# Kernel tuning notes

Measured on AMD Instinct MI355X. Metric: run time of the kernel, lower is better.

Reference implementation:

```python
import jax, jax.numpy as jnp
import numpy as np

H = 16  # num heads
D = 64  # head dim


def rotate_half(x):
    h = x.shape[-1] // 2
    return jnp.concatenate([-x[..., h:], x[..., :h]], axis=-1)


def setup_inputs() -> dict:
    key = jax.random.key(0)
    ks = jax.random.split(key, 8)
    B, S, E = 2, 4096, 1024
    scale = 1.0 / np.sqrt(E)
    x = jax.random.normal(ks[0], (B, S, E), dtype=jnp.float32)
    Wq = jax.random.normal(ks[1], (E, E), dtype=jnp.float32) * scale
    Wk = jax.random.normal(ks[2], (E, E), dtype=jnp.float32) * scale
    Wv = jax.random.normal(ks[3], (E, E), dtype=jnp.float32) * scale
    Wg = jax.random.normal(ks[4], (E, E), dtype=jnp.float32) * scale
    Wo = jax.random.normal(ks[5], (E, E), dtype=jnp.float32) * scale
    cos = jax.random.normal(ks[6], (S, D), dtype=jnp.float32)
    sin = jax.random.normal(ks[7], (S, D), dtype=jnp.float32)
    return {"x": x, "Wq": Wq, "Wk": Wk, "Wv": Wv, "Wg": Wg, "Wo": Wo,
            "cos": cos, "sin": sin, "block_size": 256}


def reference(x, Wq, Wk, Wv, Wg, Wo, cos, sin, block_size):
    B, S, E = x.shape
    nb = S // block_size  # seq divisible by block_size (remainder==0 path)

    gate = (x @ Wg).reshape(B, S, H, D)
    q = (x @ Wq).reshape(B, S, H, D)
    k = (x @ Wk).reshape(B, S, H, D)
    v = (x @ Wv).reshape(B, S, H, D)

    # RoPE: cos/sin [S, D] -> broadcast over batch and heads (unsqueeze_dim=1 in torch
    # with [S, 1, D] after slicing gives the same broadcast over the head axis here).
    c = cos[:S][None, :, None, :]  # [1, S, 1, D]
    s = sin[:S][None, :, None, :]
    q = q * c + rotate_half(q) * s
    k = k * c + rotate_half(k) * s

    # Block-diagonal attention: reshape seq into blocks and attend within blocks only.
    def to_blocks(t):  # [B,S,H,D] -> [B,nb,H,block,D]
        return t.reshape(B, nb, block_size, H, D).transpose(0, 1, 3, 2, 4)

    qb, kb, vb = to_blocks(q), to_blocks(k), to_blocks(v)
    scores = jnp.einsum('bnhqd,bnhkd->bnhqk', qb, kb) / np.sqrt(D)
    attn = jax.nn.softmax(scores, axis=-1)
    ob = jnp.einsum('bnhqk,bnhkd->bnhqd', attn, vb)

    out = ob.transpose(0, 1, 3, 2, 4).reshape(B, S, H, D)  # back to [B,S,H,D]
    out = (out * jax.nn.sigmoid(gate)).reshape(B, S, H * D)
    return out @ Wo
```

## Files before the change

kernel.cpp:

```cpp
#include <hip/hip_runtime.h>
#include <hip/hip_bf16.h>
#include <stdint.h>

typedef __bf16 bf16_t;
typedef __bf16 bf16x8 __attribute__((ext_vector_type(8)));
typedef float f32x4 __attribute__((ext_vector_type(4)));

#define DEVI __device__ __forceinline__

constexpr int BB = 2;
constexpr int SS = 4096;
constexpr int EE = 1024;
constexpr int HH = 16;
constexpr int DD = 64;
constexpr int MM = BB * SS;

DEVI void gload16(const void* g, void* l) {
  __builtin_amdgcn_global_load_lds(
      (const __attribute__((address_space(1))) void*)g,
      (__attribute__((address_space(3))) void*)l, 16, 0, 0);
}

__global__ void cvt_kernel(const float* __restrict__ in, bf16_t* __restrict__ out, int n8) {
  int i = blockIdx.x * 256 + threadIdx.x;
  if (i >= n8) return;
  const float* p = in + (size_t)i * 8;
  bf16x8 o;
#pragma unroll
  for (int j = 0; j < 8; ++j) o[j] = (bf16_t)p[j];
  *(bf16x8*)(out + (size_t)i * 8) = o;
}

__global__ void wt_kernel(const float* __restrict__ w0, const float* __restrict__ w1,
                          const float* __restrict__ w2, const float* __restrict__ w3,
                          const float* __restrict__ w4, bf16_t* __restrict__ out) {
  __shared__ float tile[32][33];
  const float* Wsel = blockIdx.z == 0 ? w0 : blockIdx.z == 1 ? w1 :
                      blockIdx.z == 2 ? w2 : blockIdx.z == 3 ? w3 : w4;
  bf16_t* O = out + (size_t)blockIdx.z * EE * EE;
  int n0 = blockIdx.x * 32, k0 = blockIdx.y * 32;
  int tx = threadIdx.x & 31, ty = threadIdx.x >> 5;
#pragma unroll
  for (int i = 0; i < 4; ++i)
    tile[ty + i * 8][tx] = Wsel[(size_t)(k0 + ty + i * 8) * EE + n0 + tx];
  __syncthreads();
#pragma unroll
  for (int i = 0; i < 4; ++i)
    O[(size_t)(n0 + ty + i * 8) * EE + k0 + tx] = (bf16_t)tile[tx][ty + i * 8];
}

template <int MODE>
__global__ __launch_bounds__(256) void gemm_bt(const bf16_t* __restrict__ A,
                                               const bf16_t* __restrict__ Bt,
                                               void* __restrict__ Cout, int Kdim) {
  __shared__ bf16_t Al[128 * 64];
  __shared__ bf16_t Bl[128 * 64];
  const int m0 = blockIdx.x * 128;
  const int n0 = blockIdx.y * 128;
  const int tid = threadIdx.x;
  const int wv = tid >> 6, ln = tid & 63;
  const int wm = wv >> 1, wn = wv & 1;
  f32x4 acc[4][4] = {};

  for (int k0 = 0; k0 < Kdim; k0 += 64) {
    __syncthreads();
#pragma unroll
    for (int i = 0; i < 4; ++i) {
      int slot = i * 256 + wv * 64 + ln;
      int r = slot >> 3, c = slot & 7;
      int cs = c ^ (r & 7);
      gload16(A + (size_t)(m0 + r) * Kdim + k0 + cs * 8, Al + (size_t)(i * 256 + wv * 64) * 8);
      gload16(Bt + (size_t)(n0 + r) * Kdim + k0 + cs * 8, Bl + (size_t)(i * 256 + wv * 64) * 8);
    }
    __syncthreads();
#pragma unroll
    for (int kk = 0; kk < 2; ++kk) {
      bf16x8 af[4], bfr[4];
#pragma unroll
      for (int mi = 0; mi < 4; ++mi) {
        int row = wm * 64 + mi * 16 + (ln & 15);
        int ch = (kk * 4 + (ln >> 4)) ^ (row & 7);
        af[mi] = *(const bf16x8*)(Al + row * 64 + ch * 8);
      }
#pragma unroll
      for (int ni = 0; ni < 4; ++ni) {
        int row = wn * 64 + ni * 16 + (ln & 15);
        int ch = (kk * 4 + (ln >> 4)) ^ (row & 7);
        bfr[ni] = *(const bf16x8*)(Bl + row * 64 + ch * 8);
      }
#pragma unroll
      for (int mi = 0; mi < 4; ++mi)
#pragma unroll
        for (int ni = 0; ni < 4; ++ni)
          acc[mi][ni] = __builtin_amdgcn_mfma_f32_16x16x32_bf16(af[mi], bfr[ni], acc[mi][ni], 0, 0, 0);
    }
  }

  if (MODE == 0) {
    bf16_t* Obase = (bf16_t*)Cout;
#pragma unroll
    for (int mi = 0; mi < 4; ++mi) {
#pragma unroll
      for (int ni = 0; ni < 4; ++ni) {
        int row = m0 + wm * 64 + mi * 16 + ((ln >> 4) << 2);
        int col = n0 + wn * 64 + ni * 16 + (ln & 15);
        int widx = col >> 10, ncol = col & 1023;
        bf16_t* W = Obase + (size_t)widx * MM * EE;
        if (widx == 2) {
          int h = ncol >> 6, d = ncol & 63;
          int b = row >> 12, s = row & (SS - 1);
          bf16_t* p = W + (((size_t)b * HH + h) * DD + d) * SS + s;
#pragma unroll
          for (int r = 0; r < 4; ++r) p[r] = (bf16_t)acc[mi][ni][r];
        } else {
          bf16_t* p = W + (size_t)row * EE + ncol;
#pragma unroll
          for (int r = 0; r < 4; ++r) p[(size_t)r * EE] = (bf16_t)acc[mi][ni][r];
        }
      }
    }
  } else {
    float* O = (float*)Cout;
#pragma unroll
    for (int mi = 0; mi < 4; ++mi)
#pragma unroll
      for (int ni = 0; ni < 4; ++ni) {
        int row = m0 + wm * 64 + mi * 16 + ((ln >> 4) << 2);
        int col = n0 + wn * 64 + ni * 16 + (ln & 15);
#pragma unroll
        for (int r = 0; r < 4; ++r) O[(size_t)(row + r) * EE + col] = acc[mi][ni][r];
      }
  }
}

__global__ __launch_bounds__(256, 2) void attn_kernel(const bf16_t* __restrict__ Q,
                                                      const bf16_t* __restrict__ Kc,
                                                      const bf16_t* __restrict__ Vt,
                                                      const bf16_t* __restrict__ G,
                                                      const float* __restrict__ cosp,
                                                      const float* __restrict__ sinp,
                                                      bf16_t* __restrict__ AO) {
  __shared__ bf16_t Kl[256 * 64];
  __shared__ bf16_t Vl[64 * 256];
  __shared__ bf16_t Pl[4][32 * 64];
  const int id = blockIdx.x;
  const int swz = (id & 7) * 128 + (id >> 3);
  const int half = swz & 1, ab = swz >> 1;
  const int h = ab & 15, sb = (ab >> 4) & 15, b = ab >> 8;
  const int tid = threadIdx.x, wv = tid >> 6, ln = tid & 63;
  const int qs0 = sb * 256 + half * 128 + wv * 32;

  {
    const bf16_t* Kbase = Kc + ((size_t)b * SS + sb * 256) * EE + h * DD;
    int kr = wv * 8 + (ln >> 3), kc8 = ln & 7;
#pragma unroll
    for (int g = 0; g < 8; ++g) {
      int r = g * 32 + kr, cs = kc8 ^ (r & 7);
      gload16(Kbase + (size_t)r * EE + cs * 8, &Kl[g * 2048 + wv * 512]);
    }
    const bf16_t* Vbase = Vt + ((size_t)b * HH + h) * DD * SS + sb * 256;
    int vr = wv * 2 + (ln >> 5), vc = ln & 31;
#pragma unroll
    for (int g = 0; g < 8; ++g) {
      int r = g * 8 + vr, cs = vc ^ ((r & 7) << 2);
      gload16(Vbase + (size_t)r * SS + cs * 8, &Vl[g * 2048 + wv * 512]);
    }
  }
  __syncthreads();

  {
    int c_ = tid & 3;
#pragma unroll
    for (int rr = 0; rr < 4; ++rr) {
      int r_ = rr * 64 + (tid >> 2);
      int ks = sb * 256 + r_;
      int chl = ((c_ ^ (r_ & 7)) << 3), chh = (((c_ ^ 4) ^ (r_ & 7)) << 3);
      bf16x8 lo8 = *(bf16x8*)&Kl[r_ * 64 + chl];
      bf16x8 hi8 = *(bf16x8*)&Kl[r_ * 64 + chh];
      float cl[8], sl[8], chv[8], shv[8];
      *(f32x4*)&cl[0] = *(const f32x4*)&cosp[ks * DD + c_ * 8];
      *(f32x4*)&cl[4] = *(const f32x4*)&cosp[ks * DD + c_ * 8 + 4];
      *(f32x4*)&chv[0] = *(const f32x4*)&cosp[ks * DD + c_ * 8 + 32];
      *(f32x4*)&chv[4] = *(const f32x4*)&cosp[ks * DD + c_ * 8 + 36];
      *(f32x4*)&sl[0] = *(const f32x4*)&sinp[ks * DD + c_ * 8];
      *(f32x4*)&sl[4] = *(const f32x4*)&sinp[ks * DD + c_ * 8 + 4];
      *(f32x4*)&shv[0] = *(const f32x4*)&sinp[ks * DD + c_ * 8 + 32];
      *(f32x4*)&shv[4] = *(const f32x4*)&sinp[ks * DD + c_ * 8 + 36];
      bf16x8 olo, ohi;
#pragma unroll
      for (int j = 0; j < 8; ++j) {
        float lo = (float)lo8[j], hi = (float)hi8[j];
        olo[j] = (bf16_t)(lo * cl[j] - hi * sl[j]);
        ohi[j] = (bf16_t)(hi * chv[j] + lo * shv[j]);
      }
      *(bf16x8*)&Kl[r_ * 64 + chl] = olo;
      *(bf16x8*)&Kl[r_ * 64 + chh] = ohi;
    }
  }

  bf16x8 qf[2][2];
  const int d0 = (ln >> 4) << 3;
#pragma unroll
  for (int mi = 0; mi < 2; ++mi) {
    int qs = qs0 + mi * 16 + (ln & 15);
    const bf16_t* qp = Q + ((size_t)b * SS + qs) * EE + h * DD;
    qf[mi][0] = *(const bf16x8*)(qp + d0);
    qf[mi][1] = *(const bf16x8*)(qp + 32 + d0);
    float cl[8], sl[8], chv[8], shv[8];
    *(f32x4*)&cl[0] = *(const f32x4*)&cosp[qs * DD + d0];
    *(f32x4*)&cl[4] = *(const f32x4*)&cosp[qs * DD + d0 + 4];
    *(f32x4*)&chv[0] = *(const f32x4*)&cosp[qs * DD + d0 + 32];
    *(f32x4*)&chv[4] = *(const f32x4*)&cosp[qs * DD + d0 + 36];
    *(f32x4*)&sl[0] = *(const f32x4*)&sinp[qs * DD + d0];
    *(f32x4*)&sl[4] = *(const f32x4*)&sinp[qs * DD + d0 + 4];
    *(f32x4*)&shv[0] = *(const f32x4*)&sinp[qs * DD + d0 + 32];
    *(f32x4*)&shv[4] = *(const f32x4*)&sinp[qs * DD + d0 + 36];
#pragma unroll
    for (int j = 0; j < 8; ++j) {
      float lo = (float)qf[mi][0][j], hi = (float)qf[mi][1][j];
      qf[mi][0][j] = (bf16_t)(lo * cl[j] - hi * sl[j]);
      qf[mi][1][j] = (bf16_t)(hi * chv[j] + lo * shv[j]);
    }
  }
  __syncthreads();

  f32x4 sc[2][16];
#pragma unroll
  for (int mi = 0; mi < 2; ++mi)
#pragma unroll
    for (int ni = 0; ni < 16; ++ni) sc[mi][ni] = f32x4{0.f, 0.f, 0.f, 0.f};
  __builtin_amdgcn_s_setprio(1);
#pragma unroll
  for (int kk = 0; kk < 2; ++kk) {
#pragma unroll
    for (int ni = 0; ni < 16; ++ni) {
      int row = ni * 16 + (ln & 15);
      int ch = (kk * 4 + (ln >> 4)) ^ (row & 7);
      bf16x8 kf = *(const bf16x8*)(&Kl[row * 64 + ch * 8]);
#pragma unroll
      for (int mi = 0; mi < 2; ++mi)
        sc[mi][ni] = __builtin_amdgcn_mfma_f32_16x16x32_bf16(qf[mi][kk], kf, sc[mi][ni], 0, 0, 0);
    }
  }
  __builtin_amdgcn_s_setprio(0);

  float lr[2][4];
#pragma unroll
  for (int mi = 0; mi < 2; ++mi) {
#pragma unroll
    for (int r = 0; r < 4; ++r) {
      float mx = -1e30f;
#pragma unroll
      for (int ni = 0; ni < 16; ++ni) mx = fmaxf(mx, sc[mi][ni][r] * 0.125f);
#pragma unroll
      for (int d = 1; d < 16; d <<= 1) mx = fmaxf(mx, __shfl_xor(mx, d));
      float rs = 0.f;
#pragma unroll
      for (int ni = 0; ni < 16; ++ni) {
        float p = __expf(sc[mi][ni][r] * 0.125f - mx);
        sc[mi][ni][r] = p;
        rs += p;
      }
#pragma unroll
      for (int d = 1; d < 16; d <<= 1) rs += __shfl_xor(rs, d);
      lr[mi][r] = rs;
    }
  }

  f32x4 o[2][4] = {};
  bf16_t* P = Pl[wv];
#pragma unroll
  for (int kc = 0; kc < 4; ++kc) {
#pragma unroll
    for (int mi = 0; mi < 2; ++mi)
#pragma unroll
      for (int nq = 0; nq < 4; ++nq)
#pragma unroll
        for (int r = 0; r < 4; ++r) {
          int row = mi * 16 + ((ln >> 4) << 2) + r;
          int col = nq * 16 + (ln & 15);
          P[row * 64 + (col ^ ((row & 7) << 3))] = (bf16_t)sc[mi][kc * 4 + nq][r];
        }
    __builtin_amdgcn_s_setprio(1);
#pragma unroll
    for (int kk = 0; kk < 2; ++kk) {
      bf16x8 pf[2], vf[4];
#pragma unroll
      for (int mi = 0; mi < 2; ++mi) {
        int row = mi * 16 + (ln & 15);
        int ch = (kk * 4 + (ln >> 4)) ^ (row & 7);
        pf[mi] = *(const bf16x8*)(P + row * 64 + ch * 8);
      }
#pragma unroll
      for (int nd = 0; nd < 4; ++nd) {
        int d = nd * 16 + (ln & 15);
        int c = (kc * 8 + kk * 4 + (ln >> 4)) ^ ((d & 7) << 2);
        vf[nd] = *(const bf16x8*)(&Vl[d * 256 + c * 8]);
      }
#pragma unroll
      for (int mi = 0; mi < 2; ++mi)
#pragma unroll
        for (int nd = 0; nd < 4; ++nd)
          o[mi][nd] = __builtin_amdgcn_mfma_f32_16x16x32_bf16(pf[mi], vf[nd], o[mi][nd], 0, 0, 0);
    }
    __builtin_amdgcn_s_setprio(0);
  }

#pragma unroll
  for (int mi = 0; mi < 2; ++mi)
#pragma unroll
    for (int r = 0; r < 4; ++r) {
      float inv = 1.f / lr[mi][r];
      int m = (int)((size_t)b * SS) + qs0 + mi * 16 + ((ln >> 4) << 2) + r;
#pragma unroll
      for (int nd = 0; nd < 4; ++nd) {
        int col = h * DD + nd * 16 + (ln & 15);
        float gv = (float)G[(size_t)m * EE + col];
        float sig = 1.f / (1.f + __expf(-gv));
        AO[(size_t)m * EE + col] = (bf16_t)((o[mi][nd][r] * inv) * sig);
      }
    }
}

extern "C" void kernel_launch(void* const* d_in, const int* in_sizes, int n_in,
                              void* d_out, int out_size, void* d_ws, size_t ws_size,
                              hipStream_t stream) {
  const float* x = (const float*)d_in[0];
  const float* Wq = (const float*)d_in[1];
  const float* Wk = (const float*)d_in[2];
  const float* Wv = (const float*)d_in[3];
  const float* Wg = (const float*)d_in[4];
  const float* Wo = (const float*)d_in[5];
  const float* cosp = (const float*)d_in[6];
  const float* sinp = (const float*)d_in[7];
  float* out = (float*)d_out;

  char* ws = (char*)d_ws;
  bf16_t* XB = (bf16_t*)(ws);
  bf16_t* WT = (bf16_t*)(ws + (16ll << 20));
  bf16_t* QB = (bf16_t*)(ws + (26ll << 20));
  bf16_t* KB = (bf16_t*)(ws + (42ll << 20));
  bf16_t* VT = (bf16_t*)(ws + (58ll << 20));
  bf16_t* GB = (bf16_t*)(ws + (74ll << 20));
  bf16_t* AO = XB;

  const int n8 = MM * EE / 8;
  cvt_kernel<<<n8 / 256, 256, 0, stream>>>(x, XB, n8);
  wt_kernel<<<dim3(32, 32, 5), 256, 0, stream>>>(Wq, Wk, Wv, Wg, Wo, WT);
  gemm_bt<0><<<dim3(MM / 128, 4 * EE / 128), 256, 0, stream>>>(XB, WT, QB, EE);
  attn_kernel<<<1024, 256, 0, stream>>>(QB, KB, VT, GB, cosp, sinp, AO);
  gemm_bt<1><<<dim3(MM / 128, EE / 128), 256, 0, stream>>>(AO, WT + (size_t)4 * EE * EE, out, EE);
}
```

Baseline: 155.6 us.

## Prefetch gate and Q before barrier, vectorize gated output store via LDS transpose

The gate values and raw Q plus its cos/sin are now loaded early, before the first barrier, so their latency overlaps the async K/V LDS loads. The epilogue no longer does scalar strided 2-byte gate reads and AO writes. It stages the MFMA output tile and the row sums in LDS, then has each lane write 32 contiguous bf16 values using 16-byte vector stores. This adds an extra barrier, LDS traffic for the transpose, and more live registers for the prefetched data.

```diff
diff --git a/kernel.cpp b/kernel.cpp
--- a/kernel.cpp
+++ b/kernel.cpp
@@ -166,7 +166,45 @@
       gload16(Vbase + (size_t)r * SS + cs * 8, &Vl[g * 2048 + wv * 512]);
     }
   }
+
+  const int erow = ln >> 1, ehf = ln & 1;
+  const int em = b * SS + qs0 + erow;
+  bf16x8 gpre[4];
+  {
+    const bf16_t* gp = G + (size_t)em * EE + h * DD + ehf * 32;
+#pragma unroll
+    for (int i = 0; i < 4; ++i) gpre[i] = *(const bf16x8*)(gp + i * 8);
+  }
+
+  bf16x8 qraw[2][2];
+  float cl[2][8], sl[2][8], chv[2][8], shv[2][8];
+  const int d0 = (ln >> 4) << 3;
+#pragma unroll
+  for (int mi = 0; mi < 2; ++mi) {
+    int qs = qs0 + mi * 16 + (ln & 15);
+    const bf16_t* qp = Q + ((size_t)b * SS + qs) * EE + h * DD;
+    qraw[mi][0] = *(const bf16x8*)(qp + d0);
+    qraw[mi][1] = *(const bf16x8*)(qp + 32 + d0);
+    *(f32x4*)&cl[mi][0] = *(const f32x4*)&cosp[qs * DD + d0];
+    *(f32x4*)&cl[mi][4] = *(const f32x4*)&cosp[qs * DD + d0 + 4];
+    *(f32x4*)&chv[mi][0] = *(const f32x4*)&cosp[qs * DD + d0 + 32];
+    *(f32x4*)&chv[mi][4] = *(const f32x4*)&cosp[qs * DD + d0 + 36];
+    *(f32x4*)&sl[mi][0] = *(const f32x4*)&sinp[qs * DD + d0];
+    *(f32x4*)&sl[mi][4] = *(const f32x4*)&sinp[qs * DD + d0 + 4];
+    *(f32x4*)&shv[mi][0] = *(const f32x4*)&sinp[qs * DD + d0 + 32];
+    *(f32x4*)&shv[mi][4] = *(const f32x4*)&sinp[qs * DD + d0 + 36];
+  }
   __syncthreads();
+
+  bf16x8 qf[2][2];
+#pragma unroll
+  for (int mi = 0; mi < 2; ++mi)
+#pragma unroll
+    for (int j = 0; j < 8; ++j) {
+      float lo = (float)qraw[mi][0][j], hi = (float)qraw[mi][1][j];
+      qf[mi][0][j] = (bf16_t)(lo * cl[mi][j] - hi * sl[mi][j]);
+      qf[mi][1][j] = (bf16_t)(hi * chv[mi][j] + lo * shv[mi][j]);
+    }
 
   {
     int c_ = tid & 3;
@@ -177,49 +215,24 @@
       int chl = ((c_ ^ (r_ & 7)) << 3), chh = (((c_ ^ 4) ^ (r_ & 7)) << 3);
       bf16x8 lo8 = *(bf16x8*)&Kl[r_ * 64 + chl];
       bf16x8 hi8 = *(bf16x8*)&Kl[r_ * 64 + chh];
-      float cl[8], sl[8], chv[8], shv[8];
-      *(f32x4*)&cl[0] = *(const f32x4*)&cosp[ks * DD + c_ * 8];
-      *(f32x4*)&cl[4] = *(const f32x4*)&cosp[ks * DD + c_ * 8 + 4];
-      *(f32x4*)&chv[0] = *(const f32x4*)&cosp[ks * DD + c_ * 8 + 32];
-      *(f32x4*)&chv[4] = *(const f32x4*)&cosp[ks * DD + c_ * 8 + 36];
-      *(f32x4*)&sl[0] = *(const f32x4*)&sinp[ks * DD + c_ * 8];
-      *(f32x4*)&sl[4] = *(const f32x4*)&sinp[ks * DD + c_ * 8 + 4];
-      *(f32x4*)&shv[0] = *(const f32x4*)&sinp[ks * DD + c_ * 8 + 32];
-      *(f32x4*)&shv[4] = *(const f32x4*)&sinp[ks * DD + c_ * 8 + 36];
+      float kc_[8], ks_[8], kch[8], ksh[8];
+      *(f32x4*)&kc_[0] = *(const f32x4*)&cosp[ks * DD + c_ * 8];
+      *(f32x4*)&kc_[4] = *(const f32x4*)&cosp[ks * DD + c_ * 8 + 4];
+      *(f32x4*)&kch[0] = *(const f32x4*)&cosp[ks * DD + c_ * 8 + 32];
+      *(f32x4*)&kch[4] = *(const f32x4*)&cosp[ks * DD + c_ * 8 + 36];
+      *(f32x4*)&ks_[0] = *(const f32x4*)&sinp[ks * DD + c_ * 8];
+      *(f32x4*)&ks_[4] = *(const f32x4*)&sinp[ks * DD + c_ * 8 + 4];
+      *(f32x4*)&ksh[0] = *(const f32x4*)&sinp[ks * DD + c_ * 8 + 32];
+      *(f32x4*)&ksh[4] = *(const f32x4*)&sinp[ks * DD + c_ * 8 + 36];
       bf16x8 olo, ohi;
 #pragma unroll
       for (int j = 0; j < 8; ++j) {
         float lo = (float)lo8[j], hi = (float)hi8[j];
-        olo[j] = (bf16_t)(lo * cl[j] - hi * sl[j]);
-        ohi[j] = (bf16_t)(hi * chv[j] + lo * shv[j]);
+        olo[j] = (bf16_t)(lo * kc_[j] - hi * ks_[j]);
+        ohi[j] = (bf16_t)(hi * kch[j] + lo * ksh[j]);
       }
       *(bf16x8*)&Kl[r_ * 64 + chl] = olo;
       *(bf16x8*)&Kl[r_ * 64 + chh] = ohi;
-    }
-  }
-
-  bf16x8 qf[2][2];
-  const int d0 = (ln >> 4) << 3;
-#pragma unroll
-  for (int mi = 0; mi < 2; ++mi) {
-    int qs = qs0 + mi * 16 + (ln & 15);
-    const bf16_t* qp = Q + ((size_t)b * SS + qs) * EE + h * DD;
-    qf[mi][0] = *(const bf16x8*)(qp + d0);
-    qf[mi][1] = *(const bf16x8*)(qp + 32 + d0);
-    float cl[8], sl[8], chv[8], shv[8];
-    *(f32x4*)&cl[0] = *(const f32x4*)&cosp[qs * DD + d0];
-    *(f32x4*)&cl[4] = *(const f32x4*)&cosp[qs * DD + d0 + 4];
-    *(f32x4*)&chv[0] = *(const f32x4*)&cosp[qs * DD + d0 + 32];
-    *(f32x4*)&chv[4] = *(const f32x4*)&cosp[qs * DD + d0 + 36];
-    *(f32x4*)&sl[0] = *(const f32x4*)&sinp[qs * DD + d0];
-    *(f32x4*)&sl[4] = *(const f32x4*)&sinp[qs * DD + d0 + 4];
-    *(f32x4*)&shv[0] = *(const f32x4*)&sinp[qs * DD + d0 + 32];
-    *(f32x4*)&shv[4] = *(const f32x4*)&sinp[qs * DD + d0 + 36];
-#pragma unroll
-    for (int j = 0; j < 8; ++j) {
-      float lo = (float)qf[mi][0][j], hi = (float)qf[mi][1][j];
-      qf[mi][0][j] = (bf16_t)(lo * cl[j] - hi * sl[j]);
-      qf[mi][1][j] = (bf16_t)(hi * chv[j] + lo * shv[j]);
     }
   }
   __syncthreads();
@@ -306,20 +319,48 @@
     __builtin_amdgcn_s_setprio(0);
   }
 
+  __syncthreads();
+  float* lrT = (float*)Pl[wv];
+  if ((ln & 15) == 0) {
+#pragma unroll
+    for (int mi = 0; mi < 2; ++mi)
+#pragma unroll
+      for (int r = 0; r < 4; ++r)
+        lrT[mi * 16 + ((ln >> 4) << 2) + r] = lr[mi][r];
+  }
+  float* T = (float*)Kl + wv * 2048;
 #pragma unroll
   for (int mi = 0; mi < 2; ++mi)
 #pragma unroll
-    for (int r = 0; r < 4; ++r) {
-      float inv = 1.f / lr[mi][r];
-      int m = (int)((size_t)b * SS) + qs0 + mi * 16 + ((ln >> 4) << 2) + r;
-#pragma unroll
-      for (int nd = 0; nd < 4; ++nd) {
-        int col = h * DD + nd * 16 + (ln & 15);
-        float gv = (float)G[(size_t)m * EE + col];
+    for (int nd = 0; nd < 4; ++nd)
+#pragma unroll
+      for (int r = 0; r < 4; ++r) {
+        int row = mi * 16 + ((ln >> 4) << 2) + r;
+        int col = nd * 16 + (ln & 15);
+        int c = col >> 2;
+        T[row * 64 + ((c ^ (row & 7)) << 2) + (col & 3)] = o[mi][nd][r];
+      }
+  {
+    float inv = 1.f / lrT[erow];
+    f32x4 ov[8];
+#pragma unroll
+    for (int j = 0; j < 8; ++j) {
+      int c = ehf * 8 + j;
+      ov[j] = *(const f32x4*)&T[erow * 64 + ((c ^ (erow & 7)) << 2)];
+    }
+    bf16_t* ap = AO + (size_t)em * EE + h * DD + ehf * 32;
+#pragma unroll
+    for (int i = 0; i < 4; ++i) {
+      bf16x8 outv;
+#pragma unroll
+      for (int j2 = 0; j2 < 8; ++j2) {
+        float gv = (float)gpre[i][j2];
         float sig = 1.f / (1.f + __expf(-gv));
-        AO[(size_t)m * EE + col] = (bf16_t)((o[mi][nd][r] * inv) * sig);
-      }
-    }
+        outv[j2] = (bf16_t)(ov[i * 2 + (j2 >> 2)][j2 & 3] * inv * sig);
+      }
+      *(bf16x8*)(ap + i * 8) = outv;
+    }
+  }
 }
 
 extern "C" void kernel_launch(void* const* d_in, const int* in_sizes, int n_in,
```

Result: no change. 155.0 us (-0.4%).
